# Kernel tuning notes

Hardware: AMD Instinct MI355X
Metric: run time of the kernel (lower is better)

Reference implementation:

```python
import jax, jax.numpy as jnp
import numpy as np
import math

HEADS = 8
HID = 32
MODES = 8
IN_CH = 4
SEQ = 32
B = 2
H = 64
W = 64


def spectral_conv(x, wr, wi):
    # x: [N, Cin, H, W]; w: [Cin, Cout, m, m] complex (low rfft2 modes only)
    n, _, h, w = x.shape
    m = wr.shape[2]
    xf = jnp.fft.rfft2(x)  # [N, Cin, H, W//2+1] complex64
    of = jnp.einsum('bixy,ioxy->boxy', xf[:, :, :m, :m], wr + 1j * wi)
    out_ft = jnp.zeros((n, wr.shape[1], h, w // 2 + 1), dtype=of.dtype)
    out_ft = out_ft.at[:, :, :m, :m].set(of)
    return jnp.fft.irfft2(out_ft, s=(h, w))


def conv1x1(x, w, b):
    # x: [N, Cin, H, W], w: [Cout, Cin], b: [Cout]
    return jnp.einsum('bchw,oc->bohw', x, w) + b[None, :, None, None]


def setup_inputs() -> dict:
    key = jax.random.key(0)
    ks = jax.random.split(key, 16)
    hd = HEADS * HID
    s = 0.02
    inp = {
        'v': jax.random.normal(ks[0], (B, SEQ, IN_CH, H, W), dtype=jnp.float32),
        'qwr': jax.random.normal(ks[1], (IN_CH, hd, MODES, MODES), dtype=jnp.float32) * s,
        'qwi': jax.random.normal(ks[2], (IN_CH, hd, MODES, MODES), dtype=jnp.float32) * s,
        'kwr': jax.random.normal(ks[3], (IN_CH, hd, MODES, MODES), dtype=jnp.float32) * s,
        'kwi': jax.random.normal(ks[4], (IN_CH, hd, MODES, MODES), dtype=jnp.float32) * s,
        'vwr': jax.random.normal(ks[5], (IN_CH, hd, MODES, MODES), dtype=jnp.float32) * s,
        'vwi': jax.random.normal(ks[6], (IN_CH, hd, MODES, MODES), dtype=jnp.float32) * s,
        'u1wr': jax.random.normal(ks[7], (hd, HID, MODES, MODES), dtype=jnp.float32) * s,
        'u1wi': jax.random.normal(ks[8], (hd, HID, MODES, MODES), dtype=jnp.float32) * s,
        'u2wr': jax.random.normal(ks[9], (HID, IN_CH, MODES, MODES), dtype=jnp.float32) * s,
        'u2wi': jax.random.normal(ks[10], (HID, IN_CH, MODES, MODES), dtype=jnp.float32) * s,
        's1w': jax.random.normal(ks[11], (HID, hd), dtype=jnp.float32) * s,
        's1b': jnp.zeros((HID,), dtype=jnp.float32),
        's2w': jax.random.normal(ks[12], (IN_CH, HID), dtype=jnp.float32) * s,
        's2b': jnp.zeros((IN_CH,), dtype=jnp.float32),
    }
    return inp


def reference(v, qwr, qwi, kwr, kwi, vwr, vwi, u1wr, u1wi, u2wr, u2wi, s1w, s1b, s2w, s2b):
    b, s, c, h, w = v.shape
    scale = 1.0 / math.sqrt(HID / HEADS)
    vr = v.reshape(b * s, c, h, w)
    embed = (b, HEADS, s, -1, h, w)  # same raw row-major reshape as torch
    q = spectral_conv(vr, qwr, qwi).reshape(embed)
    k = spectral_conv(vr, kwr, kwi).reshape(embed)
    val = spectral_conv(vr, vwr, vwi).reshape(embed)
    # inner products over channel dim, then dx^2-weighted spatial integral
    ip = jnp.einsum('bhsdrc,bhtdrc->bhstrc', q, k) * scale
    dx = 1.0 / h
    l2 = jnp.sum(ip, axis=(-2, -1)) * (dx * dx)  # [b, h, s1, s2]
    A = jax.nn.softmax(l2, axis=-1)
    u = jnp.einsum('bhst,bhtdrc->bhsdrc', A, val)
    u = jnp.transpose(u, (0, 2, 1, 3, 4, 5)).reshape(b * s, HEADS * u.shape[3], h, w)
    # SimpleFNO: gelu(conv1) + skip1, then conv2 + skip2
    x1 = jax.nn.gelu(spectral_conv(u, u1wr, u1wi), approximate=False) + conv1x1(u, s1w, s1b)
    x2 = spectral_conv(x1, u2wr, u2wi) + conv1x1(x1, s2w, s2b)
    return x2.reshape(b, s, c, h, w)
```

## Files before the change

kernel.cpp:

```cpp
#include <hip/hip_runtime.h>
#include <math.h>

#define HEADS 8
#define HIDC  32
#define MODES 8
#define IN_CH 4
#define SEQ   32
#define NS    64
#define HD    256
#define NM    64
#define NPIX  4096
#define TWO_PI_D 6.283185307179586476925286766559

__device__ __forceinline__ float2 f2(float a, float b){ return make_float2(a,b); }

__global__ __launch_bounds__(256) void prep_kernel(const float* __restrict__ qwr, const float* __restrict__ qwi,
                                                   const float* __restrict__ kwr, const float* __restrict__ kwi,
                                                   const float* __restrict__ vwr, const float* __restrict__ vwi,
                                                   const float* __restrict__ u1wr, const float* __restrict__ u1wi,
                                                   float2* __restrict__ Etab,
                                                   float2* __restrict__ G2, float* __restrict__ Gdc,
                                                   float2* __restrict__ vwT,
                                                   float4* __restrict__ u1wT){
  int bid = blockIdx.x, tid = threadIdx.x;
  if (bid == 0){
    for (int t = tid; t < 512; t += 256){
      int a = t >> 3, b = t & 7;
      double sv, cv; sincos(TWO_PI_D * ((a*b) & 63) / 64.0, &sv, &cv);
      Etab[t] = f2((float)cv, (float)sv);
    }
    return;
  }
  if (bid <= 64){
    int m = bid - 1;
    __shared__ float qsr[4][257], qsi[4][257], ksr[4][257], ksi[4][257];
    for (int k = tid; k < 1024; k += 256){
      int i = k >> 8, c = k & 255;
      size_t a = ((size_t)(i*256 + c))*64 + m;
      qsr[i][c] = qwr[a]; qsi[i][c] = qwi[a];
      ksr[i][c] = kwr[a]; ksi[i][c] = kwi[a];
    }
    __syncthreads();
    int kx = m & 7, ky = m >> 3;
    float w = (kx >= 1) ? 2.0f : ((ky >= 1) ? 0.5f : 0.0f);
    for (int e = tid; e < 1024; e += 256){
      int P = e >> 7, T = (e >> 4) & 7, i = (e >> 2) & 3, j = e & 3;
      float grr=0.f, gri=0.f, gir=0.f, gii=0.f;
      for (int d = 0; d < 32; ++d){
        float ar = qsr[i][P*32+d], ai = qsi[i][P*32+d];
        float br = ksr[j][T*32+d], bi = ksi[j][T*32+d];
        grr += ar*br; gri += ar*bi; gir += ai*br; gii += ai*bi;
      }
      G2[(size_t)(((m*8+P)*4+i)*4+j)*8 + T] = f2(w*(grr+gii), w*(gir-gri));
      if (m == 0){
        int o = ((P*4+i)*4+j)*8 + T;
        Gdc[o] = grr; Gdc[1024+o] = gri; Gdc[2048+o] = gir; Gdc[3072+o] = gii;
      }
    }
    return;
  }
  if (bid <= 320){
    int t = (bid - 65)*256 + tid;
    int m = t & 63, r = t >> 6, i = r >> 8, c = r & 255;
    vwT[((size_t)m*256 + c)*4 + i] = f2(vwr[t], vwi[t]);
    return;
  }
  {
    int t = (bid - 321)*256 + tid;
    int m = t & 63, r = t >> 6, c = r >> 5, o1 = r & 31;
    float pr = ((m & 7)==0 && m) ? 0.5f : 1.0f;
    float pi = m ? pr : 0.0f;
    float wr = u1wr[t], wi = u1wi[t];
    u1wT[((size_t)m*256 + c)*32 + o1] = make_float4(pr*wr, pi*wi, pr*wi, pi*wr);
  }
}

__global__ __launch_bounds__(512) void fwd_dft_kernel(const float* __restrict__ src,
                                                      const float2* __restrict__ Etab,
                                                      float2* __restrict__ dst){
  int f = blockIdx.x, tid = threadIdx.x;
  __shared__ float  s_fld[64*68];
  __shared__ float2 s_e[64][8];
  __shared__ float2 s_a1[64][8];
  if (tid < 512) ((float2*)s_e)[tid] = Etab[tid];
  const float4* f4 = (const float4*)(src + (size_t)f*NPIX);
  for (int k = tid; k < 1024; k += 512){
    float4 v = f4[k];
    int y = k >> 4, x4 = (k & 15)*4;
    float* row = &s_fld[y*68 + x4];
    row[0]=v.x; row[1]=v.y; row[2]=v.z; row[3]=v.w;
  }
  __syncthreads();
  {
    int y = tid >> 3, kx = tid & 7;
    const float4* row = (const float4*)&s_fld[y*68];
    float sr0=0.f, si0=0.f, sr1=0.f, si1=0.f;
    for (int x4 = 0; x4 < 8; ++x4){
      float4 v = row[x4];
      int xb = x4*4;
      float2 c0 = s_e[xb+0][kx], c1 = s_e[xb+1][kx];
      float2 c2 = s_e[xb+2][kx], c3 = s_e[xb+3][kx];
      sr0 += v.x*c0.x + v.y*c1.x + v.z*c2.x + v.w*c3.x;
      si0 -= v.x*c0.y + v.y*c1.y + v.z*c2.y + v.w*c3.y;
    }
    for (int x4 = 8; x4 < 16; ++x4){
      float4 v = row[x4];
      int xb = x4*4;
      float2 c0 = s_e[xb+0][kx], c1 = s_e[xb+1][kx];
      float2 c2 = s_e[xb+2][kx], c3 = s_e[xb+3][kx];
      sr1 += v.x*c0.x + v.y*c1.x + v.z*c2.x + v.w*c3.x;
      si1 -= v.x*c0.y + v.y*c1.y + v.z*c2.y + v.w*c3.y;
    }
    s_a1[y][kx] = f2(sr0+sr1, si0+si1);
  }
  __syncthreads();
  if (tid < 64){
    int ky = tid >> 3, kx = tid & 7;
    float sr0=0.f, si0=0.f, sr1=0.f, si1=0.f;
    for (int y = 0; y < 32; ++y){
      float2 a = s_a1[y][kx];
      float2 cs = s_e[y][ky];
      sr0 += a.x*cs.x + a.y*cs.y;
      si0 += a.y*cs.x - a.x*cs.y;
    }
    for (int y = 32; y < 64; ++y){
      float2 a = s_a1[y][kx];
      float2 cs = s_e[y][ky];
      sr1 += a.x*cs.x + a.y*cs.y;
      si1 += a.y*cs.x - a.x*cs.y;
    }
    dst[(size_t)f*NM + tid] = f2(sr0+sr1, si0+si1);
  }
}

__global__ __launch_bounds__(256) void attn_kernel(const float2* __restrict__ Vf,
                                                   const float2* __restrict__ G2,
                                                   const float* __restrict__ Gdc,
                                                   float* __restrict__ A){
  int bx = blockIdx.x;
  int s = bx & 31;
  int base = ((bx >> 8) * 32) + (((bx >> 5) & 7) * 4);
  int tid = threadIdx.x;
  int t = tid & 31, mc = tid >> 5;
  __shared__ float2 s_vf[4][IN_CH][64];
  __shared__ float  s_part[8][33];
  for (int k = tid; k < 4*IN_CH*64; k += 256){
    int m = k & 63, c = (k>>6)&3, smp = k>>8;
    s_vf[smp][c][m] = Vf[((size_t)(base+smp)*IN_CH + c)*NM + m];
  }
  __syncthreads();
  int sg = s >> 3, P = s & 7;
  int tg = t >> 3, T = t & 7;
  float acc = 0.f;
  for (int mm = 0; mm < 8; ++mm){
    int m = mc*8 + mm;
    const float2* g = G2 + (size_t)((m*8+P)*16)*8 + T;
    float sub = 0.f;
    for (int i = 0; i < 4; ++i){
      float2 a = s_vf[sg][i][m];
      for (int j = 0; j < 4; ++j){
        float2 b = s_vf[tg][j][m];
        float zr = a.x*b.x + a.y*b.y;
        float zi = a.y*b.x - a.x*b.y;
        float2 gv = g[(size_t)(i*4+j)*8];
        sub += zr*gv.x - zi*gv.y;
      }
    }
    acc += sub;
  }
  if (mc == 0){
    float sub = 0.f;
    for (int i = 0; i < 4; ++i){
      float2 a = s_vf[sg][i][0];
      for (int j = 0; j < 4; ++j){
        float2 b = s_vf[tg][j][0];
        int o = ((P*4+i)*4+j)*8 + T;
        sub += a.x*b.x*Gdc[o] - a.x*b.y*Gdc[1024+o]
             - a.y*b.x*Gdc[2048+o] + a.y*b.y*Gdc[3072+o];
      }
    }
    acc += sub;
  }
  s_part[mc][t] = acc;
  __syncthreads();
  if (tid < 32){
    float l2 = 0.f;
    for (int k = 0; k < 8; ++k) l2 += s_part[k][tid];
    l2 *= 0.5f / (4096.0f * 4096.0f);
    float mx = l2;
    for (int off = 16; off; off >>= 1) mx = fmaxf(mx, __shfl_xor(mx, off, 32));
    float e = expf(l2 - mx);
    float sm = e;
    for (int off = 16; off; off >>= 1) sm += __shfl_xor(sm, off, 32);
    A[(size_t)bx*32 + tid] = e / sm;
  }
}

__global__ __launch_bounds__(256) void uspec_kernel(const float2* __restrict__ Vf,
                                                    const float2* __restrict__ vwT,
                                                    const float* __restrict__ A,
                                                    float2* __restrict__ Uf){
  int bid = blockIdx.x;
  int mg = bid & 31, hh = (bid >> 5) & 7, b = bid >> 8;
  int m0 = mg*2;
  int nbase = b*32 + hh*4;
  int tid = threadIdx.x;
  __shared__ float2 s_vw[4][2][256];
  __shared__ float2 s_vv[4][2][256];
  __shared__ float  s_A[32][33];
  __shared__ float2 s_vf[4][4][2];
  for (int k = tid; k < 2048; k += 256){
    int mm = k >> 10, c = (k >> 2) & 255, i = k & 3;
    s_vw[i][mm][c] = vwT[(size_t)m0*1024 + k];
  }
  for (int k = tid; k < 1024; k += 256)
    s_A[k>>5][k&31] = A[(size_t)((b*8+hh)*32 + (k>>5))*32 + (k&31)];
  if (tid < 32){
    int smp = tid >> 3, i = (tid >> 1) & 3, mm = tid & 1;
    s_vf[smp][i][mm] = Vf[((size_t)(nbase+smp)*4 + i)*64 + m0 + mm];
  }
  __syncthreads();
  for (int k = tid; k < 2048; k += 256){
    int smp = k >> 9, mm = (k >> 8) & 1, c = k & 255;
    float sr = 0.f, si = 0.f;
    for (int i = 0; i < 4; ++i){
      float2 v = s_vf[smp][i][mm];
      float2 w = s_vw[i][mm][c];
      sr += v.x*w.x - v.y*w.y;
      si += v.x*w.y + v.y*w.x;
    }
    s_vv[smp][mm][c] = f2(sr, si);
  }
  __syncthreads();
  int sg = tid >> 5, d = tid & 31;
  float2 acc[4][2];
  for (int ss = 0; ss < 4; ++ss)
    for (int mm = 0; mm < 2; ++mm) acc[ss][mm] = f2(0.f, 0.f);
  for (int tt = 0; tt < 32; ++tt){
    int tg = tt >> 3, c = (tt & 7)*32 + d;
    float a0 = s_A[sg*4+0][tt], a1 = s_A[sg*4+1][tt];
    float a2 = s_A[sg*4+2][tt], a3 = s_A[sg*4+3][tt];
    for (int mm = 0; mm < 2; ++mm){
      float2 v = s_vv[tg][mm][c];
      acc[0][mm].x += a0*v.x; acc[0][mm].y += a0*v.y;
      acc[1][mm].x += a1*v.x; acc[1][mm].y += a1*v.y;
      acc[2][mm].x += a2*v.x; acc[2][mm].y += a2*v.y;
      acc[3][mm].x += a3*v.x; acc[3][mm].y += a3*v.y;
    }
  }
  for (int ss = 0; ss < 4; ++ss){
    int n = b*32 + sg*4 + ss;
    for (int mm = 0; mm < 2; ++mm)
      Uf[((size_t)n*64 + m0 + mm)*256 + hh*32 + d] = acc[ss][mm];
  }
}

__global__ __launch_bounds__(256) void mix1_kernel(const float2* __restrict__ Uf,
                                                   const float4* __restrict__ u1wT,
                                                   const float* __restrict__ s1w,
                                                   float2* __restrict__ U1f, float2* __restrict__ S1f){
  int bid = blockIdx.x;
  int mg = bid & 31, n0 = (bid >> 5)*8, m0 = mg*2;
  int tid = threadIdx.x;
  __shared__ float2 s_u[8][2][256];
  __shared__ float  s_w1[32][257];
  for (int it = 0; it < 16; ++it){
    int s = it >> 1, mm = it & 1;
    s_u[s][mm][tid] = Uf[((size_t)(n0+s)*64 + m0 + mm)*256 + tid];
  }
  for (int k = tid; k < 8192; k += 256)
    s_w1[k>>8][k&255] = s1w[k];
  __syncthreads();
  int o1 = tid & 31, mm = (tid >> 5) & 1, sh = tid >> 6;
  int m = m0 + mm, sA = sh*2, sB = sh*2+1;
  const float4* wp = u1wT + (size_t)m*8192 + o1;
  float2 au0 = f2(0,0), au1 = f2(0,0), as0 = f2(0,0), as1 = f2(0,0);
  #pragma unroll 4
  for (int c = 0; c < 256; ++c){
    float4 w = wp[(size_t)c*32];
    float sw = s_w1[o1][c];
    float2 uA = s_u[sA][mm][c];
    float2 uB = s_u[sB][mm][c];
    au0.x += uA.x*w.x - uA.y*w.y;  au0.y += uA.x*w.z + uA.y*w.w;
    au1.x += uB.x*w.x - uB.y*w.y;  au1.y += uB.x*w.z + uB.y*w.w;
    as0.x += uA.x*sw;  as0.y += uA.y*sw;
    as1.x += uB.x*sw;  as1.y += uB.y*sw;
  }
  size_t obA = ((size_t)(n0+sA)*32 + o1)*64 + m;
  size_t obB = ((size_t)(n0+sB)*32 + o1)*64 + m;
  U1f[obA] = au0; S1f[obA] = as0;
  U1f[obB] = au1; S1f[obB] = as1;
}

__global__ __launch_bounds__(512) void xg_kernel(const float2* __restrict__ Etab,
                                                 const float2* __restrict__ U1f,
                                                 float2* __restrict__ Xg){
  int f0 = blockIdx.x*2, tid = threadIdx.x;
  __shared__ float2 s_e[64][8];
  __shared__ float2 s_eT[8][64];
  __shared__ float2 s_gu[2][64];
  __shared__ float2 s_tu[2][64][8];
  __shared__ float  s_fld[2][64*68];
  if (tid < 512){
    float2 v = Etab[tid];
    int a = tid >> 3, b = tid & 7;
    s_e[a][b] = v; s_eT[b][a] = v;
  }
  if (tid < 128) ((float2*)s_gu)[tid] = U1f[(size_t)f0*NM + tid];
  __syncthreads();
  for (int o = tid; o < 1024; o += 512){
    int fl = o >> 9, r = o & 511, y = r >> 3, kx = r & 7;
    float wf = (kx ? 2.0f : 1.0f) * (1.0f/4096.0f);
    float a0=0.f, b0=0.f, a1=0.f, b1=0.f;
    for (int ky = 0; ky < 4; ++ky){
      float2 cs = s_e[y][ky];
      float2 gu = s_gu[fl][ky*8+kx];
      a0 += gu.x*cs.x - gu.y*cs.y;
      b0 += gu.x*cs.y + gu.y*cs.x;
    }
    for (int ky = 4; ky < 8; ++ky){
      float2 cs = s_e[y][ky];
      float2 gu = s_gu[fl][ky*8+kx];
      a1 += gu.x*cs.x - gu.y*cs.y;
      b1 += gu.x*cs.y + gu.y*cs.x;
    }
    s_tu[fl][y][kx] = f2((a0+a1)*wf, (b0+b1)*wf);
  }
  __syncthreads();
  int xx = tid & 63;
  float2 ce[8];
  #pragma unroll
  for (int k = 0; k < 8; ++k) ce[k] = s_eT[k][xx];
  for (int i = 0; i < 8; ++i){
    int p = i*512 + tid, y = p >> 6;
    const float4* tp0 = (const float4*)&s_tu[0][y][0];
    const float4* tp1 = (const float4*)&s_tu[1][y][0];
    float4 a0=tp0[0], a1=tp0[1], a2=tp0[2], a3=tp0[3];
    float4 b0=tp1[0], b1=tp1[1], b2=tp1[2], b3=tp1[3];
    float h0 = a0.x*ce[0].x - a0.y*ce[0].y + a0.z*ce[1].x - a0.w*ce[1].y
             + a1.x*ce[2].x - a1.y*ce[2].y + a1.z*ce[3].x - a1.w*ce[3].y;
    float h1 = a2.x*ce[4].x - a2.y*ce[4].y + a2.z*ce[5].x - a2.w*ce[5].y
             + a3.x*ce[6].x - a3.y*ce[6].y + a3.z*ce[7].x - a3.w*ce[7].y;
    float k0 = b0.x*ce[0].x - b0.y*ce[0].y + b0.z*ce[1].x - b0.w*ce[1].y
             + b1.x*ce[2].x - b1.y*ce[2].y + b1.z*ce[3].x - b1.w*ce[3].y;
    float k1 = b2.x*ce[4].x - b2.y*ce[4].y + b2.z*ce[5].x - b2.w*ce[5].y
             + b3.x*ce[6].x - b3.y*ce[6].y + b3.z*ce[7].x - b3.w*ce[7].y;
    float v0 = h0 + h1, v1 = k0 + k1;
    float ga = 0.5f * v0 * (1.0f + erff(v0 * 0.70710678f));
    float gb = 0.5f * v1 * (1.0f + erff(v1 * 0.70710678f));
    s_fld[0][y*68 + xx] = ga;
    s_fld[1][y*68 + xx] = gb;
  }
  __syncthreads();
  float2 (*s_a1)[64][8] = s_tu;
  for (int o = tid; o < 1024; o += 512){
    int fl = o >> 9, r = o & 511, y = r >> 3, kx = r & 7;
    const float4* row = (const float4*)&s_fld[fl][y*68];
    float sr0=0.f, si0=0.f, sr1=0.f, si1=0.f;
    for (int x4 = 0; x4 < 8; ++x4){
      float4 v = row[x4];
      int xb = x4*4;
      float2 c0 = s_e[xb+0][kx], c1 = s_e[xb+1][kx];
      float2 c2 = s_e[xb+2][kx], c3 = s_e[xb+3][kx];
      sr0 += v.x*c0.x + v.y*c1.x + v.z*c2.x + v.w*c3.x;
      si0 -= v.x*c0.y + v.y*c1.y + v.z*c2.y + v.w*c3.y;
    }
    for (int x4 = 8; x4 < 16; ++x4){
      float4 v = row[x4];
      int xb = x4*4;
      float2 c0 = s_e[xb+0][kx], c1 = s_e[xb+1][kx];
      float2 c2 = s_e[xb+2][kx], c3 = s_e[xb+3][kx];
      sr1 += v.x*c0.x + v.y*c1.x + v.z*c2.x + v.w*c3.x;
      si1 -= v.x*c0.y + v.y*c1.y + v.z*c2.y + v.w*c3.y;
    }
    s_a1[fl][y][kx] = f2(sr0+sr1, si0+si1);
  }
  __syncthreads();
  if (tid < 128){
    int fl = tid >> 6, t6 = tid & 63;
    int ky = t6 >> 3, kx = t6 & 7;
    float sr0=0.f, si0=0.f, sr1=0.f, si1=0.f;
    for (int y = 0; y < 32; ++y){
      float2 a = s_a1[fl][y][kx];
      float2 cs = s_e[y][ky];
      sr0 += a.x*cs.x + a.y*cs.y;
      si0 += a.y*cs.x - a.x*cs.y;
    }
    for (int y = 32; y < 64; ++y){
      float2 a = s_a1[fl][y][kx];
      float2 cs = s_e[y][ky];
      sr1 += a.x*cs.x + a.y*cs.y;
      si1 += a.y*cs.x - a.x*cs.y;
    }
    Xg[(size_t)(f0+fl)*NM + t6] = f2(sr0+sr1, si0+si1);
  }
}

__global__ __launch_bounds__(256) void final_spec_kernel(const float2* __restrict__ S1f,
                                                         const float2* __restrict__ Xg,
                                                         const float* __restrict__ u2wr, const float* __restrict__ u2wi,
                                                         const float* __restrict__ s1b,
                                                         const float* __restrict__ s2w,
                                                         float2* __restrict__ OS){
  int n = blockIdx.x, tid = threadIdx.x;
  __shared__ float s_w2[128], s_s1b[32];
  if (tid < 128) s_w2[tid] = s2w[tid];
  else if (tid < 160) s_s1b[tid-128] = s1b[tid-128];
  __syncthreads();
  int o2 = tid >> 6, m = tid & 63;
  float prm = ((m & 7)==0 && m) ? 0.5f : 1.0f;
  float pim = m ? prm : 0.0f;
  float dc = (m == 0) ? 4096.0f : 0.0f;
  float cr = 0.f, ci = 0.f;
  for (int o1 = 0; o1 < 32; ++o1){
    float2 xg = Xg[((size_t)n*32 + o1)*NM + m];
    float2 sf = S1f[((size_t)n*32 + o1)*NM + m];
    float Xr = xg.x + sf.x*prm + dc*s_s1b[o1];
    float Xi = xg.y + sf.y*pim;
    size_t wb = ((size_t)(o1*IN_CH + o2))*NM + m;
    float wr = u2wr[wb], wi = u2wi[wb];
    float sw = s_w2[o2*32 + o1];
    cr += Xr*wr - Xi*wi + sw*sf.x;
    ci += Xr*wi + Xi*wr + sw*sf.y;
  }
  OS[((size_t)n*IN_CH + o2)*NM + m] = f2(cr, ci);
}

__global__ __launch_bounds__(512) void final_kernel(const float2* __restrict__ Etab,
                                                    const float2* __restrict__ U1f,
                                                    const float2* __restrict__ OS,
                                                    const float* __restrict__ s1b,
                                                    const float* __restrict__ s2w, const float* __restrict__ s2b,
                                                    float* __restrict__ out){
  int n = blockIdx.x >> 3, tile = blockIdx.x & 7, y0 = tile*8;
  int tid = threadIdx.x;
  __shared__ float2 s_e[64][8];
  __shared__ float2 s_eT[8][64];
  __shared__ float2 s_u1[32][64];
  __shared__ float2 s_os[4][64];
  __shared__ float2 s_T[32][8][8];
  __shared__ float2 s_tmp[4][8][8];
  __shared__ float  s_w2[128], s_s1b[32], s_b2[4];
  if (tid < 512){
    float2 v = Etab[tid];
    s_e[tid>>3][tid&7] = v; s_eT[tid&7][tid>>3] = v;
  }
  for (int k = tid; k < 2048; k += 512) ((float2*)s_u1)[k] = U1f[(size_t)n*2048 + k];
  if (tid < 256) ((float2*)s_os)[tid] = OS[(size_t)n*256 + tid];
  else if (tid < 384) s_w2[tid-256] = s2w[tid-256];
  else if (tid < 416) s_s1b[tid-384] = s1b[tid-384];
  else if (tid < 420) s_b2[tid-416] = s2b[tid-416];
  __syncthreads();
  for (int e = tid; e < 2048; e += 512){
    int c = e >> 6, yy = (e >> 3) & 7, kx = e & 7;
    int y = y0 + yy;
    float wf = (kx ? 2.0f : 1.0f) * (1.0f/4096.0f);
    float ar = 0.f, ai = 0.f;
    for (int ky = 0; ky < 8; ++ky){
      float2 cs = s_e[y][ky];
      float2 g = s_u1[c][ky*8+kx];
      ar += g.x*cs.x - g.y*cs.y;
      ai += g.x*cs.y + g.y*cs.x;
    }
    s_T[c][yy][kx] = f2(ar*wf, ai*wf);
  }
  if (tid < 256){
    int o2 = tid >> 6, yy = (tid >> 3) & 7, kx = tid & 7;
    int y = y0 + yy;
    float wf = (kx ? 2.0f : 1.0f) * (1.0f/4096.0f);
    float tr=0.f, ti=0.f;
    for (int ky = 0; ky < 8; ++ky){
      float2 cs = s_e[y][ky];
      float2 g = s_os[o2][ky*8+kx];
      tr += g.x*cs.x - g.y*cs.y;
      ti += g.x*cs.y + g.y*cs.x;
    }
    s_tmp[o2][yy][kx] = f2(tr*wf, ti*wf);
  }
  __syncthreads();
  int yy = tid >> 6, xx = tid & 63;
  float2 ce[8];
  #pragma unroll
  for (int k = 0; k < 8; ++k) ce[k] = s_eT[k][xx];
  float a0 = s_b2[0], a1 = s_b2[1], a2 = s_b2[2], a3 = s_b2[3];
  for (int c = 0; c < 32; ++c){
    float b = s_s1b[c];
    a0 += s_w2[c]*b; a1 += s_w2[32+c]*b; a2 += s_w2[64+c]*b; a3 += s_w2[96+c]*b;
  }
  #pragma unroll 4
  for (int c = 0; c < 32; ++c){
    const float4* tp = (const float4*)&s_T[c][yy][0];
    float4 t0 = tp[0], t1 = tp[1], t2 = tp[2], t3 = tp[3];
    float h0 = t0.x*ce[0].x - t0.y*ce[0].y + t0.z*ce[1].x - t0.w*ce[1].y
             + t1.x*ce[2].x - t1.y*ce[2].y + t1.z*ce[3].x - t1.w*ce[3].y;
    float h1 = t2.x*ce[4].x - t2.y*ce[4].y + t2.z*ce[5].x - t2.w*ce[5].y
             + t3.x*ce[6].x - t3.y*ce[6].y + t3.z*ce[7].x - t3.w*ce[7].y;
    float vu = h0 + h1;
    float g = 0.5f * vu * (1.0f + erff(vu * 0.70710678f));
    a0 += s_w2[c]*g; a1 += s_w2[32+c]*g; a2 += s_w2[64+c]*g; a3 += s_w2[96+c]*g;
  }
  float sp[4];
  #pragma unroll
  for (int o2 = 0; o2 < 4; ++o2){
    const float4* tp = (const float4*)&s_tmp[o2][yy][0];
    float4 t0 = tp[0], t1 = tp[1], t2 = tp[2], t3 = tp[3];
    float h0 = t0.x*ce[0].x - t0.y*ce[0].y + t0.z*ce[1].x - t0.w*ce[1].y
             + t1.x*ce[2].x - t1.y*ce[2].y + t1.z*ce[3].x - t1.w*ce[3].y;
    float h1 = t2.x*ce[4].x - t2.y*ce[4].y + t2.z*ce[5].x - t2.w*ce[5].y
             + t3.x*ce[6].x - t3.y*ce[6].y + t3.z*ce[7].x - t3.w*ce[7].y;
    sp[o2] = h0 + h1;
  }
  int p = (y0 + yy)*64 + xx;
  float* ob = out + (size_t)n*IN_CH*NPIX;
  ob[p]          = a0 + sp[0];
  ob[NPIX + p]   = a1 + sp[1];
  ob[2*NPIX + p] = a2 + sp[2];
  ob[3*NPIX + p] = a3 + sp[3];
}

extern "C" void kernel_launch(void* const* d_in, const int* in_sizes, int n_in,
                              void* d_out, int out_size, void* d_ws, size_t ws_size,
                              hipStream_t stream) {
  (void)in_sizes; (void)n_in; (void)out_size; (void)ws_size;
  const float* v    = (const float*)d_in[0];
  const float* qwr  = (const float*)d_in[1];
  const float* qwi  = (const float*)d_in[2];
  const float* kwr  = (const float*)d_in[3];
  const float* kwi  = (const float*)d_in[4];
  const float* vwr  = (const float*)d_in[5];
  const float* vwi  = (const float*)d_in[6];
  const float* u1wr = (const float*)d_in[7];
  const float* u1wi = (const float*)d_in[8];
  const float* u2wr = (const float*)d_in[9];
  const float* u2wi = (const float*)d_in[10];
  const float* s1w  = (const float*)d_in[11];
  const float* s1b  = (const float*)d_in[12];
  const float* s2w  = (const float*)d_in[13];
  const float* s2b  = (const float*)d_in[14];
  float* out = (float*)d_out;

  float* ws = (float*)d_ws;
  size_t off = 0;
  float2* Etab =(float2*)(ws + off); off += 1024;
  float2* Vf   = (float2*)(ws + off); off += (size_t)NS*IN_CH*NM*2;
  float2* G2   = (float2*)(ws + off); off += (size_t)65536*2;
  float*  Gdc  =          (ws + off); off += 4096;
  float*  A    =          (ws + off); off += 16384;
  float2* Uf   = (float2*)(ws + off); off += (size_t)NS*NM*HD*2;
  float2* U1f  = (float2*)(ws + off); off += (size_t)NS*HIDC*NM*2;
  float2* S1f  = (float2*)(ws + off); off += (size_t)NS*HIDC*NM*2;
  float2* Xg   = (float2*)(ws + off); off += (size_t)NS*HIDC*NM*2;
  float4* u1wT = (float4*)(ws + off); off += (size_t)524288*4;
  float2* vwT  = (float2*)(ws + off); off += (size_t)65536*2;
  float2* OS   = (float2*)(ws + off); off += (size_t)NS*IN_CH*NM*2;

  prep_kernel<<<2369, 256, 0, stream>>>(qwr, qwi, kwr, kwi, vwr, vwi, u1wr, u1wi,
                                        Etab, G2, Gdc, vwT, u1wT);
  fwd_dft_kernel<<<NS*IN_CH, 512, 0, stream>>>(v, Etab, Vf);
  attn_kernel<<<512, 256, 0, stream>>>(Vf, G2, Gdc, A);
  uspec_kernel<<<512, 256, 0, stream>>>(Vf, vwT, A, Uf);
  mix1_kernel<<<256, 256, 0, stream>>>(Uf, u1wT, s1w, U1f, S1f);
  xg_kernel<<<1024, 512, 0, stream>>>(Etab, U1f, Xg);
  final_spec_kernel<<<NS, 256, 0, stream>>>(S1f, Xg, u2wr, u2wi, s1b, s2w, OS);
  final_kernel<<<NS*8, 512, 0, stream>>>(Etab, U1f, OS, s1b, s2w, s2b, out);
}
```

Before: 200.5 us.

## Store GELU field from xg_kernel and reuse in final_kernel; constant twiddle table

xg_kernel now writes the GELU-activated 64x64 fields to a global workspace buffer, and final_kernel reads them back. This replaces final_kernel's per-block recomputation of the inverse DFT of U1f and the erf-based GELU for all 32 channels. The runtime Etab sincos table is also replaced by a compile-time constant twiddle array, which removes the first prep block and one global load per kernel. The cost is an extra 8 MB write plus read of global memory in exchange for skipping the redundant transcendental and DFT work.

```diff
diff --git a/kernel.cpp b/kernel.cpp
--- a/kernel.cpp
+++ b/kernel.cpp
@@ -10,29 +10,54 @@
 #define HD    256
 #define NM    64
 #define NPIX  4096
-#define TWO_PI_D 6.283185307179586476925286766559
 
 __device__ __forceinline__ float2 f2(float a, float b){ return make_float2(a,b); }
+
+__device__ __constant__ float2 c_tw[64] = {
+  { 1.000000000000000f, 0.000000000000000f}, { 0.995184726672197f, 0.098017140329561f},
+  { 0.980785280403230f, 0.195090322016128f}, { 0.956940335732209f, 0.290284677254462f},
+  { 0.923879532511287f, 0.382683432365090f}, { 0.881921264348355f, 0.471396736825998f},
+  { 0.831469612302545f, 0.555570233019602f}, { 0.773010453362737f, 0.634393284163645f},
+  { 0.707106781186548f, 0.707106781186548f}, { 0.634393284163645f, 0.773010453362737f},
+  { 0.555570233019602f, 0.831469612302545f}, { 0.471396736825998f, 0.881921264348355f},
+  { 0.382683432365090f, 0.923879532511287f}, { 0.290284677254462f, 0.956940335732209f},
+  { 0.195090322016128f, 0.980785280403230f}, { 0.098017140329561f, 0.995184726672197f},
+  { 0.000000000000000f, 1.000000000000000f}, {-0.098017140329561f, 0.995184726672197f},
+  {-0.195090322016128f, 0.980785280403230f}, {-0.290284677254462f, 0.956940335732209f},
+  {-0.382683432365090f, 0.923879532511287f}, {-0.471396736825998f, 0.881921264348355f},
+  {-0.555570233019602f, 0.831469612302545f}, {-0.634393284163645f, 0.773010453362737f},
+  {-0.707106781186548f, 0.707106781186548f}, {-0.773010453362737f, 0.634393284163645f},
+  {-0.831469612302545f, 0.555570233019602f}, {-0.881921264348355f, 0.471396736825998f},
+  {-0.923879532511287f, 0.382683432365090f}, {-0.956940335732209f, 0.290284677254462f},
+  {-0.980785280403230f, 0.195090322016128f}, {-0.995184726672197f, 0.098017140329561f},
+  {-1.000000000000000f, 0.000000000000000f}, {-0.995184726672197f,-0.098017140329561f},
+  {-0.980785280403230f,-0.195090322016128f}, {-0.956940335732209f,-0.290284677254462f},
+  {-0.923879532511287f,-0.382683432365090f}, {-0.881921264348355f,-0.471396736825998f},
+  {-0.831469612302545f,-0.555570233019602f}, {-0.773010453362737f,-0.634393284163645f},
+  {-0.707106781186548f,-0.707106781186548f}, {-0.634393284163645f,-0.773010453362737f},
+  {-0.555570233019602f,-0.831469612302545f}, {-0.471396736825998f,-0.881921264348355f},
+  {-0.382683432365090f,-0.923879532511287f}, {-0.290284677254462f,-0.956940335732209f},
+  {-0.195090322016128f,-0.980785280403230f}, {-0.098017140329561f,-0.995184726672197f},
+  { 0.000000000000000f,-1.000000000000000f}, { 0.098017140329561f,-0.995184726672197f},
+  { 0.195090322016128f,-0.980785280403230f}, { 0.290284677254462f,-0.956940335732209f},
+  { 0.382683432365090f,-0.923879532511287f}, { 0.471396736825998f,-0.881921264348355f},
+  { 0.555570233019602f,-0.831469612302545f}, { 0.634393284163645f,-0.773010453362737f},
+  { 0.707106781186548f,-0.707106781186548f}, { 0.773010453362737f,-0.634393284163645f},
+  { 0.831469612302545f,-0.555570233019602f}, { 0.881921264348355f,-0.471396736825998f},
+  { 0.923879532511287f,-0.382683432365090f}, { 0.956940335732209f,-0.290284677254462f},
+  { 0.980785280403230f,-0.195090322016128f}, { 0.995184726672197f,-0.098017140329561f}
+};
 
 __global__ __launch_bounds__(256) void prep_kernel(const float* __restrict__ qwr, const float* __restrict__ qwi,
                                                    const float* __restrict__ kwr, const float* __restrict__ kwi,
                                                    const float* __restrict__ vwr, const float* __restrict__ vwi,
                                                    const float* __restrict__ u1wr, const float* __restrict__ u1wi,
-                                                   float2* __restrict__ Etab,
                                                    float2* __restrict__ G2, float* __restrict__ Gdc,
                                                    float2* __restrict__ vwT,
                                                    float4* __restrict__ u1wT){
   int bid = blockIdx.x, tid = threadIdx.x;
-  if (bid == 0){
-    for (int t = tid; t < 512; t += 256){
-      int a = t >> 3, b = t & 7;
-      double sv, cv; sincos(TWO_PI_D * ((a*b) & 63) / 64.0, &sv, &cv);
-      Etab[t] = f2((float)cv, (float)sv);
-    }
-    return;
-  }
-  if (bid <= 64){
-    int m = bid - 1;
+  if (bid < 64){
+    int m = bid;
     __shared__ float qsr[4][257], qsi[4][257], ksr[4][257], ksi[4][257];
     for (int k = tid; k < 1024; k += 256){
       int i = k >> 8, c = k & 255;
@@ -59,14 +84,14 @@
     }
     return;
   }
-  if (bid <= 320){
-    int t = (bid - 65)*256 + tid;
+  if (bid < 320){
+    int t = (bid - 64)*256 + tid;
     int m = t & 63, r = t >> 6, i = r >> 8, c = r & 255;
     vwT[((size_t)m*256 + c)*4 + i] = f2(vwr[t], vwi[t]);
     return;
   }
   {
-    int t = (bid - 321)*256 + tid;
+    int t = (bid - 320)*256 + tid;
     int m = t & 63, r = t >> 6, c = r >> 5, o1 = r & 31;
     float pr = ((m & 7)==0 && m) ? 0.5f : 1.0f;
     float pi = m ? pr : 0.0f;
@@ -76,13 +101,12 @@
 }
 
 __global__ __launch_bounds__(512) void fwd_dft_kernel(const float* __restrict__ src,
-                                                      const float2* __restrict__ Etab,
                                                       float2* __restrict__ dst){
   int f = blockIdx.x, tid = threadIdx.x;
   __shared__ float  s_fld[64*68];
   __shared__ float2 s_e[64][8];
   __shared__ float2 s_a1[64][8];
-  if (tid < 512) ((float2*)s_e)[tid] = Etab[tid];
+  { int a = tid >> 3, b = tid & 7; s_e[a][b] = c_tw[(a*b) & 63]; }
   const float4* f4 = (const float4*)(src + (size_t)f*NPIX);
   for (int k = tid; k < 1024; k += 512){
     float4 v = f4[k];
@@ -292,20 +316,16 @@
   U1f[obB] = au1; S1f[obB] = as1;
 }
 
-__global__ __launch_bounds__(512) void xg_kernel(const float2* __restrict__ Etab,
-                                                 const float2* __restrict__ U1f,
-                                                 float2* __restrict__ Xg){
+__global__ __launch_bounds__(512) void xg_kernel(const float2* __restrict__ U1f,
+                                                 float2* __restrict__ Xg,
+                                                 float* __restrict__ g){
   int f0 = blockIdx.x*2, tid = threadIdx.x;
   __shared__ float2 s_e[64][8];
   __shared__ float2 s_eT[8][64];
   __shared__ float2 s_gu[2][64];
   __shared__ float2 s_tu[2][64][8];
   __shared__ float  s_fld[2][64*68];
-  if (tid < 512){
-    float2 v = Etab[tid];
-    int a = tid >> 3, b = tid & 7;
-    s_e[a][b] = v; s_eT[b][a] = v;
-  }
+  { int a = tid >> 3, b = tid & 7; float2 v = c_tw[(a*b) & 63]; s_e[a][b] = v; s_eT[b][a] = v; }
   if (tid < 128) ((float2*)s_gu)[tid] = U1f[(size_t)f0*NM + tid];
   __syncthreads();
   for (int o = tid; o < 1024; o += 512){
@@ -331,6 +351,7 @@
   float2 ce[8];
   #pragma unroll
   for (int k = 0; k < 8; ++k) ce[k] = s_eT[k][xx];
+  float* g0p = g + (size_t)f0*NPIX;
   for (int i = 0; i < 8; ++i){
     int p = i*512 + tid, y = p >> 6;
     const float4* tp0 = (const float4*)&s_tu[0][y][0];
@@ -350,6 +371,8 @@
     float gb = 0.5f * v1 * (1.0f + erff(v1 * 0.70710678f));
     s_fld[0][y*68 + xx] = ga;
     s_fld[1][y*68 + xx] = gb;
+    g0p[p] = ga;
+    g0p[NPIX + p] = gb;
   }
   __syncthreads();
   float2 (*s_a1)[64][8] = s_tu;
@@ -426,8 +449,7 @@
   OS[((size_t)n*IN_CH + o2)*NM + m] = f2(cr, ci);
 }
 
-__global__ __launch_bounds__(512) void final_kernel(const float2* __restrict__ Etab,
-                                                    const float2* __restrict__ U1f,
+__global__ __launch_bounds__(512) void final_kernel(const float* __restrict__ g,
                                                     const float2* __restrict__ OS,
                                                     const float* __restrict__ s1b,
                                                     const float* __restrict__ s2w, const float* __restrict__ s2b,
@@ -436,34 +458,15 @@
   int tid = threadIdx.x;
   __shared__ float2 s_e[64][8];
   __shared__ float2 s_eT[8][64];
-  __shared__ float2 s_u1[32][64];
   __shared__ float2 s_os[4][64];
-  __shared__ float2 s_T[32][8][8];
   __shared__ float2 s_tmp[4][8][8];
   __shared__ float  s_w2[128], s_s1b[32], s_b2[4];
-  if (tid < 512){
-    float2 v = Etab[tid];
-    s_e[tid>>3][tid&7] = v; s_eT[tid&7][tid>>3] = v;
-  }
-  for (int k = tid; k < 2048; k += 512) ((float2*)s_u1)[k] = U1f[(size_t)n*2048 + k];
+  { int a = tid >> 3, b = tid & 7; float2 v = c_tw[(a*b) & 63]; s_e[a][b] = v; s_eT[b][a] = v; }
   if (tid < 256) ((float2*)s_os)[tid] = OS[(size_t)n*256 + tid];
   else if (tid < 384) s_w2[tid-256] = s2w[tid-256];
   else if (tid < 416) s_s1b[tid-384] = s1b[tid-384];
   else if (tid < 420) s_b2[tid-416] = s2b[tid-416];
   __syncthreads();
-  for (int e = tid; e < 2048; e += 512){
-    int c = e >> 6, yy = (e >> 3) & 7, kx = e & 7;
-    int y = y0 + yy;
-    float wf = (kx ? 2.0f : 1.0f) * (1.0f/4096.0f);
-    float ar = 0.f, ai = 0.f;
-    for (int ky = 0; ky < 8; ++ky){
-      float2 cs = s_e[y][ky];
-      float2 g = s_u1[c][ky*8+kx];
-      ar += g.x*cs.x - g.y*cs.y;
-      ai += g.x*cs.y + g.y*cs.x;
-    }
-    s_T[c][yy][kx] = f2(ar*wf, ai*wf);
-  }
   if (tid < 256){
     int o2 = tid >> 6, yy = (tid >> 3) & 7, kx = tid & 7;
     int y = y0 + yy;
@@ -471,14 +474,15 @@
     float tr=0.f, ti=0.f;
     for (int ky = 0; ky < 8; ++ky){
       float2 cs = s_e[y][ky];
-      float2 g = s_os[o2][ky*8+kx];
-      tr += g.x*cs.x - g.y*cs.y;
-      ti += g.x*cs.y + g.y*cs.x;
+      float2 gv = s_os[o2][ky*8+kx];
+      tr += gv.x*cs.x - gv.y*cs.y;
+      ti += gv.x*cs.y + gv.y*cs.x;
     }
     s_tmp[o2][yy][kx] = f2(tr*wf, ti*wf);
   }
   __syncthreads();
   int yy = tid >> 6, xx = tid & 63;
+  int p = (y0 + yy)*64 + xx;
   float2 ce[8];
   #pragma unroll
   for (int k = 0; k < 8; ++k) ce[k] = s_eT[k][xx];
@@ -487,17 +491,11 @@
     float b = s_s1b[c];
     a0 += s_w2[c]*b; a1 += s_w2[32+c]*b; a2 += s_w2[64+c]*b; a3 += s_w2[96+c]*b;
   }
-  #pragma unroll 4
+  const float* gp = g + (size_t)n*HIDC*NPIX + p;
+  #pragma unroll 8
   for (int c = 0; c < 32; ++c){
-    const float4* tp = (const float4*)&s_T[c][yy][0];
-    float4 t0 = tp[0], t1 = tp[1], t2 = tp[2], t3 = tp[3];
-    float h0 = t0.x*ce[0].x - t0.y*ce[0].y + t0.z*ce[1].x - t0.w*ce[1].y
-             + t1.x*ce[2].x - t1.y*ce[2].y + t1.z*ce[3].x - t1.w*ce[3].y;
-    float h1 = t2.x*ce[4].x - t2.y*ce[4].y + t2.z*ce[5].x - t2.w*ce[5].y
-             + t3.x*ce[6].x - t3.y*ce[6].y + t3.z*ce[7].x - t3.w*ce[7].y;
-    float vu = h0 + h1;
-    float g = 0.5f * vu * (1.0f + erff(vu * 0.70710678f));
-    a0 += s_w2[c]*g; a1 += s_w2[32+c]*g; a2 += s_w2[64+c]*g; a3 += s_w2[96+c]*g;
+    float gv = gp[(size_t)c*NPIX];
+    a0 += s_w2[c]*gv; a1 += s_w2[32+c]*gv; a2 += s_w2[64+c]*gv; a3 += s_w2[96+c]*gv;
   }
   float sp[4];
   #pragma unroll
@@ -510,7 +508,6 @@
              + t3.x*ce[6].x - t3.y*ce[6].y + t3.z*ce[7].x - t3.w*ce[7].y;
     sp[o2] = h0 + h1;
   }
-  int p = (y0 + yy)*64 + xx;
   float* ob = out + (size_t)n*IN_CH*NPIX;
   ob[p]          = a0 + sp[0];
   ob[NPIX + p]   = a1 + sp[1];
@@ -541,7 +538,6 @@
 
   float* ws = (float*)d_ws;
   size_t off = 0;
-  float2* Etab =(float2*)(ws + off); off += 1024;
   float2* Vf   = (float2*)(ws + off); off += (size_t)NS*IN_CH*NM*2;
   float2* G2   = (float2*)(ws + off); off += (size_t)65536*2;
   float*  Gdc  =          (ws + off); off += 4096;
@@ -553,14 +549,15 @@
   float4* u1wT = (float4*)(ws + off); off += (size_t)524288*4;
   float2* vwT  = (float2*)(ws + off); off += (size_t)65536*2;
   float2* OS   = (float2*)(ws + off); off += (size_t)NS*IN_CH*NM*2;
-
-  prep_kernel<<<2369, 256, 0, stream>>>(qwr, qwi, kwr, kwi, vwr, vwi, u1wr, u1wi,
-                                        Etab, G2, Gdc, vwT, u1wT);
-  fwd_dft_kernel<<<NS*IN_CH, 512, 0, stream>>>(v, Etab, Vf);
+  float*  gfld =          (ws + off); off += (size_t)NS*HIDC*NPIX;
+
+  prep_kernel<<<2368, 256, 0, stream>>>(qwr, qwi, kwr, kwi, vwr, vwi, u1wr, u1wi,
+                                        G2, Gdc, vwT, u1wT);
+  fwd_dft_kernel<<<NS*IN_CH, 512, 0, stream>>>(v, Vf);
   attn_kernel<<<512, 256, 0, stream>>>(Vf, G2, Gdc, A);
   uspec_kernel<<<512, 256, 0, stream>>>(Vf, vwT, A, Uf);
   mix1_kernel<<<256, 256, 0, stream>>>(Uf, u1wT, s1w, U1f, S1f);
-  xg_kernel<<<1024, 512, 0, stream>>>(Etab, U1f, Xg);
+  xg_kernel<<<1024, 512, 0, stream>>>(U1f, Xg, gfld);
   final_spec_kernel<<<NS, 256, 0, stream>>>(S1f, Xg, u2wr, u2wi, s1b, s2w, OS);
-  final_kernel<<<NS*8, 512, 0, stream>>>(Etab, U1f, OS, s1b, s2w, s2b, out);
-}
+  final_kernel<<<NS*8, 512, 0, stream>>>(gfld, OS, s1b, s2w, s2b, out);
+}
```

Result: faster. 196.5 us (-2.0%).
